# Kernel optimization log

Measured on AMD Instinct MI355X. Metric: run time of the kernel, lower is better.

Reference implementation:

```python
import jax, jax.numpy as jnp
import numpy as np

N_NODES = 50000
N_EDGES = 800000
HID = 128
NF = 128
EC = 100
IN_DIM = 5
N_BLOCKS = 6
CUTOFF = 10.0
LOG2 = float(np.log(2.0))


def ssp(x):
    # ShiftedSoftplus: softplus(x) - log(2)
    return jax.nn.softplus(x) - LOG2


def setup_inputs() -> dict:
    key = jax.random.key(0)
    ks = jax.random.split(key, 16)
    s = 0.05
    inp = {
        "z": jax.random.normal(ks[0], (N_NODES, IN_DIM + HID), dtype=jnp.float32),
        "edge_index": jax.random.randint(ks[1], (2, N_EDGES), 0, N_NODES, dtype=jnp.int32),
        "edge_length": jax.random.uniform(ks[2], (N_EDGES,), dtype=jnp.float32) * 12.0,
        "edge_attr": jax.random.normal(ks[3], (N_EDGES, EC), dtype=jnp.float32),
        # node embedding linear (input_dim -> hidden)
        "emblin_w": jax.random.normal(ks[4], (IN_DIM, HID), dtype=jnp.float32) * s,
        "emblin_b": jnp.zeros((HID,), dtype=jnp.float32),
        # per-block stacked params [N_BLOCKS, ...]
        "lin1_w": jax.random.normal(ks[5], (N_BLOCKS, HID, NF), dtype=jnp.float32) * s,
        "nn_w1": jax.random.normal(ks[6], (N_BLOCKS, EC, NF), dtype=jnp.float32) * s,
        "nn_b1": jnp.zeros((N_BLOCKS, NF), dtype=jnp.float32),
        "nn_w2": jax.random.normal(ks[7], (N_BLOCKS, NF, NF), dtype=jnp.float32) * s,
        "nn_b2": jnp.zeros((N_BLOCKS, NF), dtype=jnp.float32),
        "lin2_w": jax.random.normal(ks[8], (N_BLOCKS, NF, HID), dtype=jnp.float32) * s,
        "lin2_b": jnp.zeros((N_BLOCKS, HID), dtype=jnp.float32),
        "lin_w": jax.random.normal(ks[9], (N_BLOCKS, HID, HID), dtype=jnp.float32) * s,
        "lin_b": jnp.zeros((N_BLOCKS, HID), dtype=jnp.float32),
    }
    return inp


def reference(z, edge_index, edge_length, edge_attr, emblin_w, emblin_b,
              lin1_w, nn_w1, nn_b1, nn_w2, nn_b2, lin2_w, lin2_b, lin_w, lin_b):
    zf, ptemb = z[:, :IN_DIM], z[:, IN_DIM:]
    h = zf @ emblin_w + emblin_b + ptemb  # [N, HID]
    src, dst = edge_index[0], edge_index[1]
    # hard cutoff mask (smooth=False)
    C = ((edge_length <= CUTOFF) & (edge_length >= 0.0)).astype(h.dtype)[:, None]  # [E,1]
    n = h.shape[0]
    for i in range(N_BLOCKS):
        # edge filter network
        W = ssp(edge_attr @ nn_w1[i] + nn_b1[i]) @ nn_w2[i] + nn_b2[i]  # [E, NF]
        W = W * C
        x = h @ lin1_w[i]  # [N, NF], no bias
        msg = x[src] * W  # gather-multiply  [E, NF]
        agg = jax.ops.segment_sum(msg, dst, num_segments=n)  # scatter-add [N, NF]
        x = agg @ lin2_w[i] + lin2_b[i]
        x = ssp(x)
        x = x @ lin_w[i] + lin_b[i]
        h = h + x
    return h
```

## Files before the change

kernel.cpp:

```cpp
#include <hip/hip_runtime.h>
#include <cstddef>

typedef __bf16 bf16;
typedef bf16 bf16x4 __attribute__((ext_vector_type(4)));
typedef bf16 bf16x8 __attribute__((ext_vector_type(8)));
typedef float f32x4 __attribute__((ext_vector_type(4)));

#define N_NODES 50000
#define N_EDGES 800000
#define HID 128
#define NF 128
#define EC 100
#define NBLK 6
#define IN_DIM 5
#define LN2 0.69314718055994530942f
#define LDST 136
#define MST 136
#define EAS 112
#define FRAG_ELEMS 16384
#define HIST_PAD 50176

__device__ __forceinline__ float ssp_f(float v) {
  float e = __expf(-fabsf(v));
  return fmaxf(v, 0.0f) + __logf(1.0f + e) - LN2;
}

__device__ __forceinline__ f32x4 zero4() {
  f32x4 v; v[0] = 0.f; v[1] = 0.f; v[2] = 0.f; v[3] = 0.f; return v;
}

__global__ void repack_kernel(const float* __restrict__ src, bf16* __restrict__ dst,
                              int K, int srcStride) {
  const int m = blockIdx.x;
  const float* s = src + (size_t)m * srcStride;
  bf16* d = dst + (size_t)m * FRAG_ELEMS;
  const int tid = threadIdx.x;
  const int wave = tid >> 6, lane = tid & 63;
  const int quad = lane >> 4, lanelo = lane & 15;
  const int col = wave * 32 + lanelo;
#pragma unroll
  for (int nt = 0; nt < 2; nt++)
#pragma unroll
    for (int ks = 0; ks < 4; ks++) {
      bf16x8 f;
#pragma unroll
      for (int j = 0; j < 8; j++) {
        int k = ks * 32 + quad * 8 + j;
        f[j] = (bf16)((k < K) ? s[(size_t)k * 128 + col + nt * 16] : 0.0f);
      }
      *(bf16x8*)&d[(size_t)(((wave * 2 + nt) * 4 + ks) * 64 + lane) * 8] = f;
    }
}

__global__ void hist_kernel(const int* __restrict__ ei, const float* __restrict__ elen,
                            int* __restrict__ hist, int* __restrict__ nvalid) {
  int e = blockIdx.x * 256 + threadIdx.x;
  if (e < N_EDGES) {
    float L = elen[e];
    if (L <= 10.0f && L >= 0.0f) {
      atomicAdd(&hist[ei[N_EDGES + e]], 1);
      atomicAdd(nvalid, 1);
    }
  }
}

__global__ void scan_blocks_kernel(const int* __restrict__ in, int* __restrict__ out,
                                   int* __restrict__ bsums) {
  __shared__ int s[256];
  int i = blockIdx.x * 256 + threadIdx.x;
  int v = in[i];
  s[threadIdx.x] = v;
  __syncthreads();
#pragma unroll
  for (int off = 1; off < 256; off <<= 1) {
    int t = (threadIdx.x >= off) ? s[threadIdx.x - off] : 0;
    __syncthreads();
    s[threadIdx.x] += t;
    __syncthreads();
  }
  out[i] = s[threadIdx.x] - v;
  if (threadIdx.x == 255) bsums[blockIdx.x] = s[255];
}

__global__ void scan_bsums_kernel(int* __restrict__ bsums, int nb) {
  __shared__ int s[256];
  int v = (threadIdx.x < nb) ? bsums[threadIdx.x] : 0;
  s[threadIdx.x] = v;
  __syncthreads();
#pragma unroll
  for (int off = 1; off < 256; off <<= 1) {
    int t = (threadIdx.x >= off) ? s[threadIdx.x - off] : 0;
    __syncthreads();
    s[threadIdx.x] += t;
    __syncthreads();
  }
  if (threadIdx.x < nb) bsums[threadIdx.x] = s[threadIdx.x] - v;
}

__global__ void scan_add_kernel(int* __restrict__ out, const int* __restrict__ bsums,
                                int* __restrict__ cursor) {
  int i = blockIdx.x * 256 + threadIdx.x;
  int v = out[i] + bsums[blockIdx.x];
  out[i] = v;
  cursor[i] = v;
}

__global__ void scatter_kernel(const int* __restrict__ ei, const float* __restrict__ elen,
                               int* __restrict__ cursor, int* __restrict__ perm,
                               int2* __restrict__ einfo) {
  int e = blockIdx.x * 256 + threadIdx.x;
  if (e < N_EDGES) {
    float L = elen[e];
    if (L <= 10.0f && L >= 0.0f) {
      int s = ei[e];
      int d = ei[N_EDGES + e];
      int pos = atomicAdd(&cursor[d], 1);
      perm[pos] = e;
      einfo[pos] = make_int2(s, d);
    }
  }
}

__global__ void permute_ea_kernel(const float* __restrict__ ea,
                                  const int* __restrict__ perm,
                                  const int* __restrict__ nvalid,
                                  bf16* __restrict__ eas) {
  const int nv = *nvalid;
  const int e0 = blockIdx.x * 64;
  if (e0 >= nv) return;
  const int tid = threadIdx.x;
#pragma unroll
  for (int it = 0; it < 4; it++) {
    int u = tid + it * 256;
    if (u < 64 * 14) {
      int r = u / 14, s = u - r * 14;
      int row = e0 + r;
      bf16x8 o;
#pragma unroll
      for (int j = 0; j < 8; j++) o[j] = (bf16)0.0f;
      if (row < nv) {
        int pe = perm[row];
        const float* src = ea + (size_t)pe * EC;
        if (s < 12) {
          float4 a = *(const float4*)&src[s * 8];
          float4 b = *(const float4*)&src[s * 8 + 4];
          o[0] = (bf16)a.x; o[1] = (bf16)a.y; o[2] = (bf16)a.z; o[3] = (bf16)a.w;
          o[4] = (bf16)b.x; o[5] = (bf16)b.y; o[6] = (bf16)b.z; o[7] = (bf16)b.w;
        } else if (s == 12) {
          float4 a = *(const float4*)&src[96];
          o[0] = (bf16)a.x; o[1] = (bf16)a.y; o[2] = (bf16)a.z; o[3] = (bf16)a.w;
        }
      }
      *(bf16x8*)&eas[(size_t)row * EAS + s * 8] = o;
    }
  }
}

__global__ void embed_kernel(const float* __restrict__ z,
                             const float* __restrict__ ew,
                             const float* __restrict__ eb,
                             float* __restrict__ h) {
  int i = blockIdx.x * 256 + threadIdx.x;
  if (i >= N_NODES * HID) return;
  int n = i >> 7, c = i & 127;
  const float* zr = z + (size_t)n * (IN_DIM + HID);
  float acc = eb[c] + zr[IN_DIM + c];
#pragma unroll
  for (int k = 0; k < IN_DIM; k++) acc = fmaf(zr[k], ew[k * HID + c], acc);
  h[i] = acc;
}

__global__ void zero_kernel(float4* __restrict__ p, int n4) {
  int i = blockIdx.x * 256 + threadIdx.x;
  if (i < n4) p[i] = make_float4(0.f, 0.f, 0.f, 0.f);
}

__global__ __launch_bounds__(256, 4)
void xgemm_kernel(const float* __restrict__ hmat,
                  const bf16* __restrict__ wf,
                  float* __restrict__ xout) {
  __shared__ bf16 sA[64 * LDST];
  const int tid = threadIdx.x;
  const int wave = tid >> 6, lane = tid & 63;
  const int quad = lane >> 4, lanelo = lane & 15;
  const int ncol0 = wave * 32;
  const int row0 = blockIdx.x * 64;

  bf16x8 Bf[2][4];
#pragma unroll
  for (int nt = 0; nt < 2; nt++)
#pragma unroll
    for (int ks = 0; ks < 4; ks++)
      Bf[nt][ks] = *(const bf16x8*)&wf[(size_t)(((wave * 2 + nt) * 4 + ks) * 64 + lane) * 8];

#pragma unroll
  for (int it = 0; it < 8; it++) {
    int idx = tid + it * 256;
    int r = idx >> 5, c4 = idx & 31;
    int grow = row0 + r;
    float4 v = (grow < N_NODES) ? *(const float4*)&hmat[(size_t)grow * HID + c4 * 4]
                                : make_float4(0.f, 0.f, 0.f, 0.f);
    bf16x4 o; o[0] = (bf16)v.x; o[1] = (bf16)v.y; o[2] = (bf16)v.z; o[3] = (bf16)v.w;
    *(bf16x4*)&sA[r * LDST + c4 * 4] = o;
  }
  __syncthreads();

  f32x4 acc[4][2];
#pragma unroll
  for (int mt = 0; mt < 4; mt++)
#pragma unroll
    for (int nt = 0; nt < 2; nt++) acc[mt][nt] = zero4();
#pragma unroll
  for (int ks = 0; ks < 4; ks++) {
    bf16x8 a[4];
#pragma unroll
    for (int mt = 0; mt < 4; mt++)
      a[mt] = *(const bf16x8*)&sA[(mt * 16 + lanelo) * LDST + ks * 32 + quad * 8];
#pragma unroll
    for (int mt = 0; mt < 4; mt++)
#pragma unroll
      for (int nt = 0; nt < 2; nt++)
        acc[mt][nt] = __builtin_amdgcn_mfma_f32_16x16x32_bf16(a[mt], Bf[nt][ks], acc[mt][nt], 0, 0, 0);
  }
#pragma unroll
  for (int mt = 0; mt < 4; mt++)
#pragma unroll
    for (int r = 0; r < 4; r++) {
      int grow = row0 + mt * 16 + quad * 4 + r;
      if (grow < N_NODES) {
#pragma unroll
        for (int nt = 0; nt < 2; nt++)
          xout[(size_t)grow * NF + ncol0 + nt * 16 + lanelo] = acc[mt][nt][r];
      }
    }
}

__global__ __launch_bounds__(256, 4)
void edge_kernel(const bf16* __restrict__ eas,
                 const int2* __restrict__ einfo,
                 const int* __restrict__ nvalid,
                 const bf16* __restrict__ w1f, const float* __restrict__ b1,
                 const bf16* __restrict__ w2f, const float* __restrict__ b2,
                 const float* __restrict__ x,
                 float* __restrict__ agg) {
  __shared__ alignas(16) char s_buf[64 * MST * 4];
  bf16* sA = (bf16*)s_buf;
  float* s_msg = (float*)s_buf;
  __shared__ int s_src[64];
  __shared__ int s_dst[64];

  const int nv = *nvalid;
  const int e0 = blockIdx.x * 64;
  if (e0 >= nv) return;

  const int tid = threadIdx.x;
  const int wave = tid >> 6, lane = tid & 63;
  const int quad = lane >> 4, lanelo = lane & 15;
  const int ncol0 = wave * 32;

  bf16x8 Bf1[2][4], Bf2[2][4];
#pragma unroll
  for (int nt = 0; nt < 2; nt++)
#pragma unroll
    for (int ks = 0; ks < 4; ks++) {
      size_t fo = (size_t)(((wave * 2 + nt) * 4 + ks) * 64 + lane) * 8;
      Bf1[nt][ks] = *(const bf16x8*)&w1f[fo];
      Bf2[nt][ks] = *(const bf16x8*)&w2f[fo];
    }
  float bias1[2], bias2[2];
#pragma unroll
  for (int nt = 0; nt < 2; nt++) {
    bias1[nt] = b1[ncol0 + nt * 16 + lanelo];
    bias2[nt] = b2[ncol0 + nt * 16 + lanelo];
  }

#pragma unroll
  for (int it = 0; it < 5; it++) {
    int u = tid + it * 256;
    if (u < 64 * 17) {
      int r = u / 17, s = u - r * 17;
      bf16x8 o;
      if (s < 14) {
        o = *(const bf16x8*)&eas[(size_t)(e0 + r) * EAS + s * 8];
      } else {
#pragma unroll
        for (int j = 0; j < 8; j++) o[j] = (bf16)0.0f;
      }
      *(bf16x8*)&sA[r * LDST + s * 8] = o;
    }
  }
  if (tid < 64) {
    int2 sd = einfo[e0 + tid];
    s_src[tid] = sd.x;
    s_dst[tid] = sd.y;
  }
  __syncthreads();

  f32x4 acc[4][2];
#pragma unroll
  for (int mt = 0; mt < 4; mt++)
#pragma unroll
    for (int nt = 0; nt < 2; nt++) acc[mt][nt] = zero4();
#pragma unroll
  for (int ks = 0; ks < 4; ks++) {
    bf16x8 a[4];
#pragma unroll
    for (int mt = 0; mt < 4; mt++)
      a[mt] = *(const bf16x8*)&sA[(mt * 16 + lanelo) * LDST + ks * 32 + quad * 8];
#pragma unroll
    for (int mt = 0; mt < 4; mt++)
#pragma unroll
      for (int nt = 0; nt < 2; nt++)
        acc[mt][nt] = __builtin_amdgcn_mfma_f32_16x16x32_bf16(a[mt], Bf1[nt][ks], acc[mt][nt], 0, 0, 0);
  }
  __syncthreads();

#pragma unroll
  for (int mt = 0; mt < 4; mt++)
#pragma unroll
    for (int nt = 0; nt < 2; nt++)
#pragma unroll
      for (int r = 0; r < 4; r++) {
        float v = ssp_f(acc[mt][nt][r] + bias1[nt]);
        sA[(mt * 16 + quad * 4 + r) * LDST + ncol0 + nt * 16 + lanelo] = (bf16)v;
      }
  __syncthreads();

#pragma unroll
  for (int mt = 0; mt < 4; mt++)
#pragma unroll
    for (int nt = 0; nt < 2; nt++) acc[mt][nt] = zero4();
#pragma unroll
  for (int ks = 0; ks < 4; ks++) {
    bf16x8 a[4];
#pragma unroll
    for (int mt = 0; mt < 4; mt++)
      a[mt] = *(const bf16x8*)&sA[(mt * 16 + lanelo) * LDST + ks * 32 + quad * 8];
#pragma unroll
    for (int mt = 0; mt < 4; mt++)
#pragma unroll
      for (int nt = 0; nt < 2; nt++)
        acc[mt][nt] = __builtin_amdgcn_mfma_f32_16x16x32_bf16(a[mt], Bf2[nt][ks], acc[mt][nt], 0, 0, 0);
  }
  __syncthreads();

#pragma unroll
  for (int mt = 0; mt < 4; mt++)
#pragma unroll
    for (int r = 0; r < 4; r++) {
      int row = mt * 16 + quad * 4 + r;
      bool valid = (e0 + row < nv);
      int srcn = s_src[row];
#pragma unroll
      for (int nt = 0; nt < 2; nt++) {
        int col = ncol0 + nt * 16 + lanelo;
        float g = valid ? x[(size_t)srcn * NF + col] : 0.0f;
        float wv = acc[mt][nt][r] + bias2[nt];
        s_msg[row * MST + col] = valid ? wv * g : 0.0f;
      }
    }
  __syncthreads();

  {
    const int col = tid & 127;
    const int r0 = (tid >> 7) * 32;
    float acc2 = 0.0f;
    int prev = s_dst[r0];
    for (int r = r0; r < r0 + 32; r++) {
      int d = s_dst[r];
      if (d != prev) {
        atomicAdd(&agg[(size_t)prev * NF + col], acc2);
        acc2 = 0.0f;
        prev = d;
      }
      acc2 += s_msg[r * MST + col];
    }
    atomicAdd(&agg[(size_t)prev * NF + col], acc2);
  }
}

__global__ __launch_bounds__(256, 4)
void node_kernel(const float* __restrict__ agg,
                 const bf16* __restrict__ w1f, const float* __restrict__ b1,
                 const bf16* __restrict__ w2f, const float* __restrict__ b2,
                 const bf16* __restrict__ wxf,
                 float* __restrict__ h,
                 float* __restrict__ x) {
  __shared__ bf16 sA[64 * LDST];
  const int tid = threadIdx.x;
  const int wave = tid >> 6, lane = tid & 63;
  const int quad = lane >> 4, lanelo = lane & 15;
  const int ncol0 = wave * 32;
  const int row0 = blockIdx.x * 64;

  bf16x8 Bf1[2][4], Bf2[2][4];
#pragma unroll
  for (int nt = 0; nt < 2; nt++)
#pragma unroll
    for (int ks = 0; ks < 4; ks++) {
      size_t fo = (size_t)(((wave * 2 + nt) * 4 + ks) * 64 + lane) * 8;
      Bf1[nt][ks] = *(const bf16x8*)&w1f[fo];
      Bf2[nt][ks] = *(const bf16x8*)&w2f[fo];
    }
  float bias1[2], bias2[2];
#pragma unroll
  for (int nt = 0; nt < 2; nt++) {
    bias1[nt] = b1[ncol0 + nt * 16 + lanelo];
    bias2[nt] = b2[ncol0 + nt * 16 + lanelo];
  }

#pragma unroll
  for (int it = 0; it < 8; it++) {
    int idx = tid + it * 256;
    int r = idx >> 5, c4 = idx & 31;
    int grow = row0 + r;
    float4 v = (grow < N_NODES) ? *(const float4*)&agg[(size_t)grow * NF + c4 * 4]
                                : make_float4(0.f, 0.f, 0.f, 0.f);
    bf16x4 o; o[0] = (bf16)v.x; o[1] = (bf16)v.y; o[2] = (bf16)v.z; o[3] = (bf16)v.w;
    *(bf16x4*)&sA[r * LDST + c4 * 4] = o;
  }
  __syncthreads();

  f32x4 acc[4][2];
#pragma unroll
  for (int mt = 0; mt < 4; mt++)
#pragma unroll
    for (int nt = 0; nt < 2; nt++) acc[mt][nt] = zero4();
#pragma unroll
  for (int ks = 0; ks < 4; ks++) {
    bf16x8 a[4];
#pragma unroll
    for (int mt = 0; mt < 4; mt++)
      a[mt] = *(const bf16x8*)&sA[(mt * 16 + lanelo) * LDST + ks * 32 + quad * 8];
#pragma unroll
    for (int mt = 0; mt < 4; mt++)
#pragma unroll
      for (int nt = 0; nt < 2; nt++)
        acc[mt][nt] = __builtin_amdgcn_mfma_f32_16x16x32_bf16(a[mt], Bf1[nt][ks], acc[mt][nt], 0, 0, 0);
  }
  __syncthreads();

#pragma unroll
  for (int mt = 0; mt < 4; mt++)
#pragma unroll
    for (int nt = 0; nt < 2; nt++)
#pragma unroll
      for (int r = 0; r < 4; r++) {
        float v = ssp_f(acc[mt][nt][r] + bias1[nt]);
        sA[(mt * 16 + quad * 4 + r) * LDST + ncol0 + nt * 16 + lanelo] = (bf16)v;
      }
  __syncthreads();

#pragma unroll
  for (int mt = 0; mt < 4; mt++)
#pragma unroll
    for (int nt = 0; nt < 2; nt++) acc[mt][nt] = zero4();
#pragma unroll
  for (int ks = 0; ks < 4; ks++) {
    bf16x8 a[4];
#pragma unroll
    for (int mt = 0; mt < 4; mt++)
      a[mt] = *(const bf16x8*)&sA[(mt * 16 + lanelo) * LDST + ks * 32 + quad * 8];
#pragma unroll
    for (int mt = 0; mt < 4; mt++)
#pragma unroll
      for (int nt = 0; nt < 2; nt++)
        acc[mt][nt] = __builtin_amdgcn_mfma_f32_16x16x32_bf16(a[mt], Bf2[nt][ks], acc[mt][nt], 0, 0, 0);
  }
  __syncthreads();

#pragma unroll
  for (int mt = 0; mt < 4; mt++)
#pragma unroll
    for (int nt = 0; nt < 2; nt++)
#pragma unroll
      for (int r = 0; r < 4; r++) {
        int row = mt * 16 + quad * 4 + r;
        int grow = row0 + row;
        int col = ncol0 + nt * 16 + lanelo;
        float hv = acc[mt][nt][r] + bias2[nt];
        if (grow < N_NODES) {
          size_t off = (size_t)grow * HID + col;
          hv += h[off];
          h[off] = hv;
        }
        sA[row * LDST + col] = (bf16)hv;
      }

  if (wxf != nullptr) {
    bf16x8 Bfx[2][4];
#pragma unroll
    for (int nt = 0; nt < 2; nt++)
#pragma unroll
      for (int ks = 0; ks < 4; ks++)
        Bfx[nt][ks] = *(const bf16x8*)&wxf[(size_t)(((wave * 2 + nt) * 4 + ks) * 64 + lane) * 8];
    __syncthreads();
#pragma unroll
    for (int mt = 0; mt < 4; mt++)
#pragma unroll
      for (int nt = 0; nt < 2; nt++) acc[mt][nt] = zero4();
#pragma unroll
    for (int ks = 0; ks < 4; ks++) {
      bf16x8 a[4];
#pragma unroll
      for (int mt = 0; mt < 4; mt++)
        a[mt] = *(const bf16x8*)&sA[(mt * 16 + lanelo) * LDST + ks * 32 + quad * 8];
#pragma unroll
      for (int mt = 0; mt < 4; mt++)
#pragma unroll
        for (int nt = 0; nt < 2; nt++)
          acc[mt][nt] = __builtin_amdgcn_mfma_f32_16x16x32_bf16(a[mt], Bfx[nt][ks], acc[mt][nt], 0, 0, 0);
    }
#pragma unroll
    for (int mt = 0; mt < 4; mt++)
#pragma unroll
      for (int r = 0; r < 4; r++) {
        int grow = row0 + mt * 16 + quad * 4 + r;
        if (grow < N_NODES) {
#pragma unroll
          for (int nt = 0; nt < 2; nt++)
            x[(size_t)grow * NF + ncol0 + nt * 16 + lanelo] = acc[mt][nt][r];
        }
      }
  }
}

extern "C" void kernel_launch(void* const* d_in, const int* in_sizes, int n_in,
                              void* d_out, int out_size, void* d_ws, size_t ws_size,
                              hipStream_t stream) {
  const float* z        = (const float*)d_in[0];
  const int*   ei       = (const int*)d_in[1];
  const float* elen     = (const float*)d_in[2];
  const float* ea       = (const float*)d_in[3];
  const float* emblin_w = (const float*)d_in[4];
  const float* emblin_b = (const float*)d_in[5];
  const float* lin1_w   = (const float*)d_in[6];
  const float* nn_w1    = (const float*)d_in[7];
  const float* nn_b1    = (const float*)d_in[8];
  const float* nn_w2    = (const float*)d_in[9];
  const float* nn_b2    = (const float*)d_in[10];
  const float* lin2_w   = (const float*)d_in[11];
  const float* lin2_b   = (const float*)d_in[12];
  const float* lin_w    = (const float*)d_in[13];
  const float* lin_b    = (const float*)d_in[14];

  float* h   = (float*)d_out;
  char* base = (char*)d_ws;
  float* x    = (float*)base;  base += (size_t)N_NODES * NF * 4;
  float* agg  = (float*)base;  base += (size_t)N_NODES * NF * 4;
  bf16* wp    = (bf16*)base;   base += (size_t)5 * NBLK * FRAG_ELEMS * 2;
  int* hist   = (int*)base;    base += (size_t)HIST_PAD * 4;
  int* cursor = (int*)base;    base += (size_t)HIST_PAD * 4;
  int* bsums  = (int*)base;    base += 1024;
  int* nvalid = (int*)base;    base += 16;
  int* perm   = (int*)base;    base += (size_t)N_EDGES * 4;
  int2* einfo = (int2*)base;   base += (size_t)N_EDGES * 8;
  bf16* eas   = (bf16*)base;   base += (size_t)N_EDGES * EAS * 2;

  bf16* wp_lin1 = wp;
  bf16* wp_nw1  = wp + 1 * (size_t)NBLK * FRAG_ELEMS;
  bf16* wp_nw2  = wp + 2 * (size_t)NBLK * FRAG_ELEMS;
  bf16* wp_l2   = wp + 3 * (size_t)NBLK * FRAG_ELEMS;
  bf16* wp_l    = wp + 4 * (size_t)NBLK * FRAG_ELEMS;

  repack_kernel<<<NBLK, 256, 0, stream>>>(lin1_w, wp_lin1, HID, HID * NF);
  repack_kernel<<<NBLK, 256, 0, stream>>>(nn_w1, wp_nw1, EC, EC * NF);
  repack_kernel<<<NBLK, 256, 0, stream>>>(nn_w2, wp_nw2, NF, NF * NF);
  repack_kernel<<<NBLK, 256, 0, stream>>>(lin2_w, wp_l2, NF, NF * HID);
  repack_kernel<<<NBLK, 256, 0, stream>>>(lin_w, wp_l, HID, HID * HID);

  const int nb = HIST_PAD / 256;
  zero_kernel<<<(HIST_PAD / 4 + 255) / 256, 256, 0, stream>>>((float4*)hist, HIST_PAD / 4);
  zero_kernel<<<1, 256, 0, stream>>>((float4*)nvalid, 1);
  zero_kernel<<<(N_EDGES * 2 / 4 + 255) / 256, 256, 0, stream>>>((float4*)einfo, N_EDGES * 2 / 4);
  hist_kernel<<<(N_EDGES + 255) / 256, 256, 0, stream>>>(ei, elen, hist, nvalid);
  scan_blocks_kernel<<<nb, 256, 0, stream>>>(hist, hist, bsums);
  scan_bsums_kernel<<<1, 256, 0, stream>>>(bsums, nb);
  scan_add_kernel<<<nb, 256, 0, stream>>>(hist, bsums, cursor);
  scatter_kernel<<<(N_EDGES + 255) / 256, 256, 0, stream>>>(ei, elen, cursor, perm, einfo);
  permute_ea_kernel<<<N_EDGES / 64, 256, 0, stream>>>(ea, perm, nvalid, eas);

  embed_kernel<<<(N_NODES * HID + 255) / 256, 256, 0, stream>>>(z, emblin_w, emblin_b, h);

  const int node_tiles = (N_NODES + 63) / 64;
  const int edge_tiles = N_EDGES / 64;

  xgemm_kernel<<<node_tiles, 256, 0, stream>>>(h, wp_lin1, x);

  for (int i = 0; i < NBLK; i++) {
    zero_kernel<<<(N_NODES * NF / 4 + 255) / 256, 256, 0, stream>>>((float4*)agg, N_NODES * NF / 4);
    edge_kernel<<<edge_tiles, 256, 0, stream>>>(eas, einfo, nvalid,
        wp_nw1 + (size_t)i * FRAG_ELEMS, nn_b1 + (size_t)i * NF,
        wp_nw2 + (size_t)i * FRAG_ELEMS, nn_b2 + (size_t)i * NF,
        x, agg);
    node_kernel<<<node_tiles, 256, 0, stream>>>(agg,
        wp_l2 + (size_t)i * FRAG_ELEMS, lin2_b + (size_t)i * HID,
        wp_l + (size_t)i * FRAG_ELEMS, lin_b + (size_t)i * HID,
        (i + 1 < NBLK) ? (wp_lin1 + (size_t)(i + 1) * FRAG_ELEMS) : nullptr,
        h, x);
  }
}
```

Before: 2.003 ms.

## Scatter edge attributes by rank, fuse embed into xgemm, prefetch source gathers

The preprocessing now records each edge's destination rank and writes bf16 edge attributes directly to their sorted slot. This replaces the gather through a perm array with coalesced reads of the fp32 input. The embedding computation is fused into the first lin1 GEMM kernel, which drops one full pass over h. In the edge kernel, the x[src] gathers are issued at kernel start into registers so their latency overlaps the weight loads and MFMA work, at the cost of extra register pressure. Rows past nvalid now get explicit validity guards.

```diff
diff --git a/kernel.cpp b/kernel.cpp
--- a/kernel.cpp
+++ b/kernel.cpp
@@ -106,68 +106,53 @@
 }
 
 __global__ void scatter_kernel(const int* __restrict__ ei, const float* __restrict__ elen,
-                               int* __restrict__ cursor, int* __restrict__ perm,
+                               int* __restrict__ cursor, int* __restrict__ rank,
                                int2* __restrict__ einfo) {
   int e = blockIdx.x * 256 + threadIdx.x;
   if (e < N_EDGES) {
     float L = elen[e];
+    int rk = -1;
     if (L <= 10.0f && L >= 0.0f) {
       int s = ei[e];
       int d = ei[N_EDGES + e];
-      int pos = atomicAdd(&cursor[d], 1);
-      perm[pos] = e;
-      einfo[pos] = make_int2(s, d);
-    }
+      rk = atomicAdd(&cursor[d], 1);
+      einfo[rk] = make_int2(s, d);
+    }
+    rank[e] = rk;
   }
 }
 
 __global__ void permute_ea_kernel(const float* __restrict__ ea,
-                                  const int* __restrict__ perm,
-                                  const int* __restrict__ nvalid,
+                                  const int* __restrict__ rank,
                                   bf16* __restrict__ eas) {
-  const int nv = *nvalid;
+  __shared__ int s_rk[64];
   const int e0 = blockIdx.x * 64;
-  if (e0 >= nv) return;
   const int tid = threadIdx.x;
+  if (tid < 64) s_rk[tid] = rank[e0 + tid];
+  __syncthreads();
 #pragma unroll
   for (int it = 0; it < 4; it++) {
     int u = tid + it * 256;
     if (u < 64 * 14) {
       int r = u / 14, s = u - r * 14;
-      int row = e0 + r;
+      int rk = s_rk[r];
+      if (rk < 0) continue;
+      const float* src = ea + (size_t)(e0 + r) * EC;
       bf16x8 o;
 #pragma unroll
       for (int j = 0; j < 8; j++) o[j] = (bf16)0.0f;
-      if (row < nv) {
-        int pe = perm[row];
-        const float* src = ea + (size_t)pe * EC;
-        if (s < 12) {
-          float4 a = *(const float4*)&src[s * 8];
-          float4 b = *(const float4*)&src[s * 8 + 4];
-          o[0] = (bf16)a.x; o[1] = (bf16)a.y; o[2] = (bf16)a.z; o[3] = (bf16)a.w;
-          o[4] = (bf16)b.x; o[5] = (bf16)b.y; o[6] = (bf16)b.z; o[7] = (bf16)b.w;
-        } else if (s == 12) {
-          float4 a = *(const float4*)&src[96];
-          o[0] = (bf16)a.x; o[1] = (bf16)a.y; o[2] = (bf16)a.z; o[3] = (bf16)a.w;
-        }
-      }
-      *(bf16x8*)&eas[(size_t)row * EAS + s * 8] = o;
-    }
-  }
-}
-
-__global__ void embed_kernel(const float* __restrict__ z,
-                             const float* __restrict__ ew,
-                             const float* __restrict__ eb,
-                             float* __restrict__ h) {
-  int i = blockIdx.x * 256 + threadIdx.x;
-  if (i >= N_NODES * HID) return;
-  int n = i >> 7, c = i & 127;
-  const float* zr = z + (size_t)n * (IN_DIM + HID);
-  float acc = eb[c] + zr[IN_DIM + c];
-#pragma unroll
-  for (int k = 0; k < IN_DIM; k++) acc = fmaf(zr[k], ew[k * HID + c], acc);
-  h[i] = acc;
+      if (s < 12) {
+        float4 a = *(const float4*)&src[s * 8];
+        float4 b = *(const float4*)&src[s * 8 + 4];
+        o[0] = (bf16)a.x; o[1] = (bf16)a.y; o[2] = (bf16)a.z; o[3] = (bf16)a.w;
+        o[4] = (bf16)b.x; o[5] = (bf16)b.y; o[6] = (bf16)b.z; o[7] = (bf16)b.w;
+      } else if (s == 12) {
+        float4 a = *(const float4*)&src[96];
+        o[0] = (bf16)a.x; o[1] = (bf16)a.y; o[2] = (bf16)a.z; o[3] = (bf16)a.w;
+      }
+      *(bf16x8*)&eas[(size_t)rk * EAS + s * 8] = o;
+    }
+  }
 }
 
 __global__ void zero_kernel(float4* __restrict__ p, int n4) {
@@ -176,9 +161,12 @@
 }
 
 __global__ __launch_bounds__(256, 4)
-void xgemm_kernel(const float* __restrict__ hmat,
-                  const bf16* __restrict__ wf,
-                  float* __restrict__ xout) {
+void embed_xgemm_kernel(const float* __restrict__ z,
+                        const float* __restrict__ ew,
+                        const float* __restrict__ eb,
+                        const bf16* __restrict__ wf,
+                        float* __restrict__ h,
+                        float* __restrict__ x) {
   __shared__ bf16 sA[64 * LDST];
   const int tid = threadIdx.x;
   const int wave = tid >> 6, lane = tid & 63;
@@ -198,9 +186,23 @@
     int idx = tid + it * 256;
     int r = idx >> 5, c4 = idx & 31;
     int grow = row0 + r;
-    float4 v = (grow < N_NODES) ? *(const float4*)&hmat[(size_t)grow * HID + c4 * 4]
-                                : make_float4(0.f, 0.f, 0.f, 0.f);
-    bf16x4 o; o[0] = (bf16)v.x; o[1] = (bf16)v.y; o[2] = (bf16)v.z; o[3] = (bf16)v.w;
+    float hv[4] = {0.f, 0.f, 0.f, 0.f};
+    if (grow < N_NODES) {
+      const float* zr = z + (size_t)grow * (IN_DIM + HID);
+      float zf[IN_DIM];
+#pragma unroll
+      for (int k = 0; k < IN_DIM; k++) zf[k] = zr[k];
+#pragma unroll
+      for (int j = 0; j < 4; j++) {
+        int c = c4 * 4 + j;
+        float acc = eb[c] + zr[IN_DIM + c];
+#pragma unroll
+        for (int k = 0; k < IN_DIM; k++) acc = fmaf(zf[k], ew[k * HID + c], acc);
+        hv[j] = acc;
+        h[(size_t)grow * HID + c] = acc;
+      }
+    }
+    bf16x4 o; o[0] = (bf16)hv[0]; o[1] = (bf16)hv[1]; o[2] = (bf16)hv[2]; o[3] = (bf16)hv[3];
     *(bf16x4*)&sA[r * LDST + c4 * 4] = o;
   }
   __syncthreads();
@@ -230,7 +232,7 @@
       if (grow < N_NODES) {
 #pragma unroll
         for (int nt = 0; nt < 2; nt++)
-          xout[(size_t)grow * NF + ncol0 + nt * 16 + lanelo] = acc[mt][nt][r];
+          x[(size_t)grow * NF + ncol0 + nt * 16 + lanelo] = acc[mt][nt][r];
       }
     }
 }
@@ -246,7 +248,6 @@
   __shared__ alignas(16) char s_buf[64 * MST * 4];
   bf16* sA = (bf16*)s_buf;
   float* s_msg = (float*)s_buf;
-  __shared__ int s_src[64];
   __shared__ int s_dst[64];
 
   const int nv = *nvalid;
@@ -257,6 +258,23 @@
   const int wave = tid >> 6, lane = tid & 63;
   const int quad = lane >> 4, lanelo = lane & 15;
   const int ncol0 = wave * 32;
+
+  float xg[4][4][2];
+  bool vld[4][4];
+#pragma unroll
+  for (int mt = 0; mt < 4; mt++)
+#pragma unroll
+    for (int r = 0; r < 4; r++) {
+      int row = mt * 16 + quad * 4 + r;
+      int2 sd = einfo[e0 + row];
+      bool v = (e0 + row) < nv;
+      vld[mt][r] = v;
+#pragma unroll
+      for (int nt = 0; nt < 2; nt++) {
+        float g = x[(size_t)sd.x * NF + ncol0 + nt * 16 + lanelo];
+        xg[mt][r][nt] = v ? g : 0.0f;
+      }
+    }
 
   bf16x8 Bf1[2][4], Bf2[2][4];
 #pragma unroll
@@ -280,7 +298,7 @@
     if (u < 64 * 17) {
       int r = u / 17, s = u - r * 17;
       bf16x8 o;
-      if (s < 14) {
+      if (s < 14 && (e0 + r) < nv) {
         o = *(const bf16x8*)&eas[(size_t)(e0 + r) * EAS + s * 8];
       } else {
 #pragma unroll
@@ -289,11 +307,7 @@
       *(bf16x8*)&sA[r * LDST + s * 8] = o;
     }
   }
-  if (tid < 64) {
-    int2 sd = einfo[e0 + tid];
-    s_src[tid] = sd.x;
-    s_dst[tid] = sd.y;
-  }
+  if (tid < 64) s_dst[tid] = einfo[e0 + tid].y;
   __syncthreads();
 
   f32x4 acc[4][2];
@@ -349,14 +363,11 @@
 #pragma unroll
     for (int r = 0; r < 4; r++) {
       int row = mt * 16 + quad * 4 + r;
-      bool valid = (e0 + row < nv);
-      int srcn = s_src[row];
 #pragma unroll
       for (int nt = 0; nt < 2; nt++) {
         int col = ncol0 + nt * 16 + lanelo;
-        float g = valid ? x[(size_t)srcn * NF + col] : 0.0f;
         float wv = acc[mt][nt][r] + bias2[nt];
-        s_msg[row * MST + col] = valid ? wv * g : 0.0f;
+        s_msg[row * MST + col] = vld[mt][r] ? wv * xg[mt][r][nt] : 0.0f;
       }
     }
   __syncthreads();
@@ -553,7 +564,7 @@
   int* cursor = (int*)base;    base += (size_t)HIST_PAD * 4;
   int* bsums  = (int*)base;    base += 1024;
   int* nvalid = (int*)base;    base += 16;
-  int* perm   = (int*)base;    base += (size_t)N_EDGES * 4;
+  int* rank   = (int*)base;    base += (size_t)N_EDGES * 4;
   int2* einfo = (int2*)base;   base += (size_t)N_EDGES * 8;
   bf16* eas   = (bf16*)base;   base += (size_t)N_EDGES * EAS * 2;
 
@@ -577,15 +588,13 @@
   scan_blocks_kernel<<<nb, 256, 0, stream>>>(hist, hist, bsums);
   scan_bsums_kernel<<<1, 256, 0, stream>>>(bsums, nb);
   scan_add_kernel<<<nb, 256, 0, stream>>>(hist, bsums, cursor);
-  scatter_kernel<<<(N_EDGES + 255) / 256, 256, 0, stream>>>(ei, elen, cursor, perm, einfo);
-  permute_ea_kernel<<<N_EDGES / 64, 256, 0, stream>>>(ea, perm, nvalid, eas);
-
-  embed_kernel<<<(N_NODES * HID + 255) / 256, 256, 0, stream>>>(z, emblin_w, emblin_b, h);
+  scatter_kernel<<<(N_EDGES + 255) / 256, 256, 0, stream>>>(ei, elen, cursor, rank, einfo);
+  permute_ea_kernel<<<N_EDGES / 64, 256, 0, stream>>>(ea, rank, eas);
 
   const int node_tiles = (N_NODES + 63) / 64;
   const int edge_tiles = N_EDGES / 64;
 
-  xgemm_kernel<<<node_tiles, 256, 0, stream>>>(h, wp_lin1, x);
+  embed_xgemm_kernel<<<node_tiles, 256, 0, stream>>>(z, emblin_w, emblin_b, wp_lin1, h, x);
 
   for (int i = 0; i < NBLK; i++) {
     zero_kernel<<<(N_NODES * NF / 4 + 255) / 256, 256, 0, stream>>>((float4*)agg, N_NODES * NF / 4);
```

Result: no change. 1.964 ms (-1.9%).
